# Optimization experiments

Hardware: AMD Instinct MI355X
Metric: run time of the kernel (lower is better)

The kernel has to match this reference:

```python
import jax, jax.numpy as jnp
from jax import lax
import numpy as np

B, T, I, H = 256, 512, 512, 1024

def setup_inputs() -> dict:
    key = jax.random.key(0)
    ks = jax.random.split(key, 6)
    s_ih = 1.0 / np.sqrt(H)
    return {
        "x": jax.random.normal(ks[0], (B, T, I), dtype=jnp.float32),
        "W_ih": jax.random.uniform(ks[1], (4 * H, I), minval=-s_ih, maxval=s_ih, dtype=jnp.float32),
        "W_hh": jax.random.uniform(ks[2], (4 * H, H), minval=-s_ih, maxval=s_ih, dtype=jnp.float32),
        "b_ih": jax.random.uniform(ks[3], (4 * H,), minval=-s_ih, maxval=s_ih, dtype=jnp.float32),
        "b_hh": jax.random.uniform(ks[4], (4 * H,), minval=-s_ih, maxval=s_ih, dtype=jnp.float32),
        "c0": jax.random.normal(ks[5], (B, H), dtype=jnp.float32),  # torch code inits cell state with randn
    }

def reference(x, W_ih, W_hh, b_ih, b_hh, c0):
    # Faithful to LSTMBody.forward: h0 = zeros, c0 = randn (provided as input),
    # per-step nn.LSTMCell; returns the final CELL state (the torch code's `out`).
    h0 = jnp.zeros((x.shape[0], W_hh.shape[1]), dtype=x.dtype)
    Wi_T = W_ih.T  # [I, 4H]
    Wh_T = W_hh.T  # [H, 4H]
    b = b_ih + b_hh

    def step(carry, xt):
        h, c = carry
        gates = xt @ Wi_T + h @ Wh_T + b  # [B, 4H]
        i, f, g, o = jnp.split(gates, 4, axis=-1)  # PyTorch gate order: i, f, g, o
        c_new = jax.nn.sigmoid(f) * c + jax.nn.sigmoid(i) * jnp.tanh(g)
        h_new = jax.nn.sigmoid(o) * jnp.tanh(c_new)
        return (h_new, c_new), None

    xs = jnp.swapaxes(x, 0, 1)  # [T, B, I] for scan over time
    (h, c), _ = lax.scan(step, (h0, c0), xs)
    return c
```

## Files before the change

### kernel.cpp

```cpp
#include <hip/hip_runtime.h>
#include <stdint.h>

#define Bsz 256
#define Tsz 512
#define Isz 512
#define Hsz 1024

typedef __attribute__((ext_vector_type(8))) short short8;
typedef __attribute__((ext_vector_type(4))) float f32x4;

static constexpr size_t XBF_OFF  = 0;
static constexpr size_t WIBF_OFF = 134217728;
static constexpr size_t HBUF_OFF = 138412032;
static constexpr size_t FLAG_OFF = 139460608;
static constexpr size_t WS_NEED  = 139493376;

__device__ __forceinline__ unsigned short f2bf(float f) {
  union { float f; unsigned u; } v; v.f = f;
  unsigned r = v.u + 0x7fff + ((v.u >> 16) & 1);
  return (unsigned short)(r >> 16);
}

__device__ __forceinline__ void cvt8(const float* __restrict__ s, unsigned short* __restrict__ d) {
  float4 a = *(const float4*)s;
  float4 b = *(const float4*)(s + 4);
  union { unsigned short us[8]; uint4 v; } o;
  o.us[0] = f2bf(a.x); o.us[1] = f2bf(a.y); o.us[2] = f2bf(a.z); o.us[3] = f2bf(a.w);
  o.us[4] = f2bf(b.x); o.us[5] = f2bf(b.y); o.us[6] = f2bf(b.z); o.us[7] = f2bf(b.w);
  *(uint4*)d = o.v;
}

__device__ __forceinline__ short8 ld_h(const unsigned short* p) {
  unsigned long long lo = __hip_atomic_load((unsigned long long*)(void*)p,
                                            __ATOMIC_RELAXED, __HIP_MEMORY_SCOPE_AGENT);
  unsigned long long hi = __hip_atomic_load((unsigned long long*)(void*)(p + 4),
                                            __ATOMIC_RELAXED, __HIP_MEMORY_SCOPE_AGENT);
  union { unsigned long long q[2]; short8 s; } u;
  u.q[0] = lo; u.q[1] = hi;
  return u.s;
}

__device__ __forceinline__ unsigned ld_flag(const unsigned* p) {
  return __hip_atomic_load((unsigned*)p, __ATOMIC_RELAXED, __HIP_MEMORY_SCOPE_AGENT);
}

__global__ __launch_bounds__(256)
void init_kernel(const float* __restrict__ x, const float* __restrict__ Wi,
                 unsigned char* __restrict__ ws)
{
  unsigned short* xbf  = (unsigned short*)(ws + XBF_OFF);
  unsigned short* wibf = (unsigned short*)(ws + WIBF_OFF);
  const int bid = blockIdx.x;
  const int tid = threadIdx.x;

  if (bid < 32768) {
    const int rowid = bid * 4 + (tid >> 6);
    const int t = rowid >> 8;
    const int b = rowid & 255;
    const int i = (tid & 63) * 8;
    const float* src = x + ((size_t)b * Tsz + t) * Isz + i;
    unsigned short* dst = xbf + (size_t)rowid * Isz + i;
    cvt8(src, dst);
  } else if (bid < 32768 + 1024) {
    const size_t base = (size_t)(bid - 32768) * 2048 + (size_t)tid * 8;
    cvt8(Wi + base, wibf + base);
  } else {
    const int z = bid - 33792;
    uint4 zero = make_uint4(0u, 0u, 0u, 0u);
    for (size_t j = (size_t)z * 256 + tid; j < 67584; j += (size_t)260 * 256)
      ((uint4*)(ws + HBUF_OFF))[j] = zero;
  }
}

__global__ __launch_bounds__(256, 1)
void lstm_persistent(const float* __restrict__ Wh,
                     const float* __restrict__ b_ih, const float* __restrict__ b_hh,
                     const float* __restrict__ c0, float* __restrict__ out,
                     unsigned char* __restrict__ ws)
{
  const unsigned short* __restrict__ xbf  = (const unsigned short*)(ws + XBF_OFF);
  const unsigned short* __restrict__ wibf = (const unsigned short*)(ws + WIBF_OFF);
  unsigned short* __restrict__ hbuf = (unsigned short*)(ws + HBUF_OFF);
  unsigned* __restrict__ flags = (unsigned*)(ws + FLAG_OFF);

  __shared__ unsigned short WhT[64][1032];
  __shared__ float bias[64];

  const int tid  = threadIdx.x;
  const int bid  = blockIdx.x;
  const int cg   = bid & 63;
  const int rg   = bid >> 6;
  const int wv   = tid >> 6;
  const int lane = tid & 63;
  const int l16  = lane & 15;
  const int quad = lane >> 4;

  {
    const int n  = tid >> 2;
    const int q  = n >> 4, u = n & 15;
    const int gc = q * 1024 + cg * 16 + u;
    const int k0 = (tid & 3) * 256;
    const float* src = Wh + (size_t)gc * Hsz + k0;
    unsigned short* dst = &WhT[n][k0];
    #pragma unroll 4
    for (int k = 0; k < 256; k += 8) cvt8(src + k, dst + k);
  }
  if (tid < 64) {
    const int q = tid >> 4, u = tid & 15;
    const int gc = q * 1024 + cg * 16 + u;
    bias[tid] = b_ih[gc] + b_hh[gc];
  }
  __syncthreads();

  const int rowbase = rg * 64 + wv * 16;
  const int arow    = rowbase + l16;
  const int hcol    = cg * 16 + l16;

  unsigned* const flag_base = flags + (size_t)rg * 2048 + (size_t)wv * 8;
  unsigned* const myslot    = flag_base + (size_t)cg * 32;
  unsigned* const pollp     = flag_base + (size_t)lane * 32;

  const float bi_r = bias[l16];
  const float bf_r = bias[16 + l16];
  const float bg_r = bias[32 + l16];
  const float bo_r = bias[48 + l16];

  float creg[4];
  #pragma unroll
  for (int r = 0; r < 4; ++r)
    creg[r] = c0[(size_t)(rowbase + quad * 4 + r) * Hsz + hcol];

  const unsigned short* bp[4];
  #pragma unroll
  for (int q = 0; q < 4; ++q)
    bp[q] = wibf + (size_t)(q * 1024 + cg * 16 + l16) * Isz + quad * 8;

  int p = 0;
  for (int t = 0; t < Tsz; ++t) {
    const unsigned short* xt = xbf  + (size_t)t * Bsz * Isz + (size_t)arow * Isz + quad * 8;
    const unsigned short* hp = hbuf + (size_t)p * Bsz * Hsz + (size_t)arow * Hsz + quad * 8;
    const unsigned tgt = (unsigned)t;

    f32x4 acc[4];
    #pragma unroll
    for (int q = 0; q < 4; ++q) acc[q] = (f32x4){0.f, 0.f, 0.f, 0.f};

    #pragma unroll 4
    for (int ks = 0; ks < 16; ++ks) {
      const int kk = ks * 32;
      short8 av = *(const short8*)(xt + kk);
      short8 b0 = *(const short8*)(bp[0] + kk);
      short8 b1 = *(const short8*)(bp[1] + kk);
      short8 b2 = *(const short8*)(bp[2] + kk);
      short8 b3 = *(const short8*)(bp[3] + kk);
      acc[0] = __builtin_amdgcn_mfma_f32_16x16x32_bf16(av, b0, acc[0], 0, 0, 0);
      acc[1] = __builtin_amdgcn_mfma_f32_16x16x32_bf16(av, b1, acc[1], 0, 0, 0);
      acc[2] = __builtin_amdgcn_mfma_f32_16x16x32_bf16(av, b2, acc[2], 0, 0, 0);
      acc[3] = __builtin_amdgcn_mfma_f32_16x16x32_bf16(av, b3, acc[3], 0, 0, 0);
    }

    if (t > 0) {
      unsigned v = ld_flag(pollp);
      while (!__all((int)(v >= tgt))) v = ld_flag(pollp);
      __atomic_signal_fence(__ATOMIC_SEQ_CST);
    }

    short8 hv[16];
    #pragma unroll
    for (int j = 0; j < 16; ++j) hv[j] = ld_h(hp + j * 32);

    #pragma unroll
    for (int ks = 0; ks < 32; ++ks) {
      short8 av = hv[ks & 15];
      if (ks + 16 < 32) hv[ks & 15] = ld_h(hp + (ks + 16) * 32);
      const int kk = ks * 32;
      short8 b0 = *(const short8*)(&WhT[l16     ][kk + quad * 8]);
      short8 b1 = *(const short8*)(&WhT[16 + l16][kk + quad * 8]);
      short8 b2 = *(const short8*)(&WhT[32 + l16][kk + quad * 8]);
      short8 b3 = *(const short8*)(&WhT[48 + l16][kk + quad * 8]);
      acc[0] = __builtin_amdgcn_mfma_f32_16x16x32_bf16(av, b0, acc[0], 0, 0, 0);
      acc[1] = __builtin_amdgcn_mfma_f32_16x16x32_bf16(av, b1, acc[1], 0, 0, 0);
      acc[2] = __builtin_amdgcn_mfma_f32_16x16x32_bf16(av, b2, acc[2], 0, 0, 0);
      acc[3] = __builtin_amdgcn_mfma_f32_16x16x32_bf16(av, b3, acc[3], 0, 0, 0);
    }

    unsigned short* hn = hbuf + (size_t)(p ^ 1) * Bsz * Hsz;
    #pragma unroll
    for (int r = 0; r < 4; ++r) {
      float gi = acc[0][r] + bi_r;
      float gf = acc[1][r] + bf_r;
      float gg = acc[2][r] + bg_r;
      float go = acc[3][r] + bo_r;
      float si = 1.f / (1.f + __expf(-gi));
      float sf = 1.f / (1.f + __expf(-gf));
      float tg = 1.f - 2.f / (__expf(2.f * gg) + 1.f);
      float so = 1.f / (1.f + __expf(-go));
      float cn = sf * creg[r] + si * tg;
      creg[r] = cn;
      float tc = 1.f - 2.f / (__expf(2.f * cn) + 1.f);
      __hip_atomic_store(&hn[(size_t)(rowbase + quad * 4 + r) * Hsz + hcol],
                         f2bf(so * tc), __ATOMIC_RELAXED, __HIP_MEMORY_SCOPE_AGENT);
    }

    asm volatile("s_waitcnt vmcnt(0)" ::: "memory");
    if (lane == 0)
      __hip_atomic_store(myslot, tgt + 1u, __ATOMIC_RELAXED, __HIP_MEMORY_SCOPE_AGENT);
    p ^= 1;
  }

  #pragma unroll
  for (int r = 0; r < 4; ++r)
    out[(size_t)(rowbase + quad * 4 + r) * Hsz + hcol] = creg[r];
}

extern "C" void kernel_launch(void* const* d_in, const int* in_sizes, int n_in,
                              void* d_out, int out_size, void* d_ws, size_t ws_size,
                              hipStream_t stream) {
  const float* x   = (const float*)d_in[0];
  const float* Wi  = (const float*)d_in[1];
  const float* Wh  = (const float*)d_in[2];
  const float* bih = (const float*)d_in[3];
  const float* bhh = (const float*)d_in[4];
  const float* c0  = (const float*)d_in[5];
  float* out = (float*)d_out;
  unsigned char* ws = (unsigned char*)d_ws;

  if (ws_size < WS_NEED) return;

  init_kernel<<<34052, 256, 0, stream>>>(x, Wi, ws);

  void* args[] = { (void*)&Wh, (void*)&bih, (void*)&bhh,
                   (void*)&c0, (void*)&out, (void*)&ws };
  hipLaunchCooperativeKernel((void*)lstm_persistent, dim3(256), dim3(256),
                             args, 0, stream);
}
```

Before: 9.934 ms.

## Split K dimension across two wave groups per block with LDS reduction

Doubles the block to 512 threads and has the second set of four waves handle the upper half of the K dimension for both the input and recurrent matmuls. Partial accumulators are reduced through shared memory, and only the first half then applies the gate nonlinearities, writes h and signals flags. This shortens the per-step serial MFMA chain inside the recurrence critical path. The cost is two block barriers per timestep plus extra LDS traffic and register pressure.

```diff
diff --git a/kernel.cpp b/kernel.cpp
--- a/kernel.cpp
+++ b/kernel.cpp
@@ -72,7 +72,7 @@
   }
 }
 
-__global__ __launch_bounds__(256, 1)
+__global__ __launch_bounds__(512, 2)
 void lstm_persistent(const float* __restrict__ Wh,
                      const float* __restrict__ b_ih, const float* __restrict__ b_hh,
                      const float* __restrict__ c0, float* __restrict__ out,
@@ -84,26 +84,29 @@
   unsigned* __restrict__ flags = (unsigned*)(ws + FLAG_OFF);
 
   __shared__ unsigned short WhT[64][1032];
+  __shared__ float red[4][64][17];
   __shared__ float bias[64];
 
   const int tid  = threadIdx.x;
   const int bid  = blockIdx.x;
   const int cg   = bid & 63;
   const int rg   = bid >> 6;
-  const int wv   = tid >> 6;
+  const int wv    = tid >> 6;
+  const int wv4   = wv & 3;
+  const int khalf = wv >> 2;
   const int lane = tid & 63;
   const int l16  = lane & 15;
   const int quad = lane >> 4;
 
   {
-    const int n  = tid >> 2;
+    const int n  = tid >> 3;
     const int q  = n >> 4, u = n & 15;
     const int gc = q * 1024 + cg * 16 + u;
-    const int k0 = (tid & 3) * 256;
+    const int k0 = (tid & 7) * 128;
     const float* src = Wh + (size_t)gc * Hsz + k0;
     unsigned short* dst = &WhT[n][k0];
     #pragma unroll 4
-    for (int k = 0; k < 256; k += 8) cvt8(src + k, dst + k);
+    for (int k = 0; k < 128; k += 8) cvt8(src + k, dst + k);
   }
   if (tid < 64) {
     const int q = tid >> 4, u = tid & 15;
@@ -112,41 +115,45 @@
   }
   __syncthreads();
 
-  const int rowbase = rg * 64 + wv * 16;
+  const int rowbase = rg * 64 + wv4 * 16;
   const int arow    = rowbase + l16;
   const int hcol    = cg * 16 + l16;
 
-  unsigned* const flag_base = flags + (size_t)rg * 2048 + (size_t)wv * 8;
+  unsigned* const flag_base = flags + (size_t)rg * 2048 + (size_t)wv4 * 8;
   unsigned* const myslot    = flag_base + (size_t)cg * 32;
-  unsigned* const pollp     = flag_base + (size_t)lane * 32;
+  unsigned* const pollp     = flag_base + (size_t)(khalf * 32 + (lane & 31)) * 32;
 
   const float bi_r = bias[l16];
   const float bf_r = bias[16 + l16];
   const float bg_r = bias[32 + l16];
   const float bo_r = bias[48 + l16];
 
-  float creg[4];
-  #pragma unroll
-  for (int r = 0; r < 4; ++r)
-    creg[r] = c0[(size_t)(rowbase + quad * 4 + r) * Hsz + hcol];
+  float creg[4] = {0.f, 0.f, 0.f, 0.f};
+  if (khalf == 0) {
+    #pragma unroll
+    for (int r = 0; r < 4; ++r)
+      creg[r] = c0[(size_t)(rowbase + quad * 4 + r) * Hsz + hcol];
+  }
 
   const unsigned short* bp[4];
   #pragma unroll
   for (int q = 0; q < 4; ++q)
-    bp[q] = wibf + (size_t)(q * 1024 + cg * 16 + l16) * Isz + quad * 8;
+    bp[q] = wibf + (size_t)(q * 1024 + cg * 16 + l16) * Isz + khalf * 256 + quad * 8;
 
   int p = 0;
   for (int t = 0; t < Tsz; ++t) {
-    const unsigned short* xt = xbf  + (size_t)t * Bsz * Isz + (size_t)arow * Isz + quad * 8;
-    const unsigned short* hp = hbuf + (size_t)p * Bsz * Hsz + (size_t)arow * Hsz + quad * 8;
+    const unsigned short* xt = xbf  + (size_t)t * Bsz * Isz + (size_t)arow * Isz
+                                    + khalf * 256 + quad * 8;
+    const unsigned short* hp = hbuf + (size_t)p * Bsz * Hsz + (size_t)arow * Hsz
+                                    + khalf * 512 + quad * 8;
     const unsigned tgt = (unsigned)t;
 
     f32x4 acc[4];
     #pragma unroll
     for (int q = 0; q < 4; ++q) acc[q] = (f32x4){0.f, 0.f, 0.f, 0.f};
 
-    #pragma unroll 4
-    for (int ks = 0; ks < 16; ++ks) {
+    #pragma unroll
+    for (int ks = 0; ks < 8; ++ks) {
       const int kk = ks * 32;
       short8 av = *(const short8*)(xt + kk);
       short8 b0 = *(const short8*)(bp[0] + kk);
@@ -165,15 +172,16 @@
       __atomic_signal_fence(__ATOMIC_SEQ_CST);
     }
 
-    short8 hv[16];
-    #pragma unroll
-    for (int j = 0; j < 16; ++j) hv[j] = ld_h(hp + j * 32);
-
-    #pragma unroll
-    for (int ks = 0; ks < 32; ++ks) {
-      short8 av = hv[ks & 15];
-      if (ks + 16 < 32) hv[ks & 15] = ld_h(hp + (ks + 16) * 32);
-      const int kk = ks * 32;
+    short8 hv[8];
+    #pragma unroll
+    for (int j = 0; j < 8; ++j) hv[j] = ld_h(hp + j * 32);
+
+    const int kbase = khalf * 512;
+    #pragma unroll
+    for (int ks = 0; ks < 16; ++ks) {
+      short8 av = hv[ks & 7];
+      if (ks + 8 < 16) hv[ks & 7] = ld_h(hp + (ks + 8) * 32);
+      const int kk = kbase + ks * 32;
       short8 b0 = *(const short8*)(&WhT[l16     ][kk + quad * 8]);
       short8 b1 = *(const short8*)(&WhT[16 + l16][kk + quad * 8]);
       short8 b2 = *(const short8*)(&WhT[32 + l16][kk + quad * 8]);
@@ -184,33 +192,54 @@
       acc[3] = __builtin_amdgcn_mfma_f32_16x16x32_bf16(av, b3, acc[3], 0, 0, 0);
     }
 
-    unsigned short* hn = hbuf + (size_t)(p ^ 1) * Bsz * Hsz;
-    #pragma unroll
-    for (int r = 0; r < 4; ++r) {
-      float gi = acc[0][r] + bi_r;
-      float gf = acc[1][r] + bf_r;
-      float gg = acc[2][r] + bg_r;
-      float go = acc[3][r] + bo_r;
-      float si = 1.f / (1.f + __expf(-gi));
-      float sf = 1.f / (1.f + __expf(-gf));
-      float tg = 1.f - 2.f / (__expf(2.f * gg) + 1.f);
-      float so = 1.f / (1.f + __expf(-go));
-      float cn = sf * creg[r] + si * tg;
-      creg[r] = cn;
-      float tc = 1.f - 2.f / (__expf(2.f * cn) + 1.f);
-      __hip_atomic_store(&hn[(size_t)(rowbase + quad * 4 + r) * Hsz + hcol],
-                         f2bf(so * tc), __ATOMIC_RELAXED, __HIP_MEMORY_SCOPE_AGENT);
-    }
-
-    asm volatile("s_waitcnt vmcnt(0)" ::: "memory");
-    if (lane == 0)
-      __hip_atomic_store(myslot, tgt + 1u, __ATOMIC_RELAXED, __HIP_MEMORY_SCOPE_AGENT);
+    if (khalf) {
+      #pragma unroll
+      for (int q = 0; q < 4; ++q)
+        #pragma unroll
+        for (int r = 0; r < 4; ++r)
+          red[wv4][lane][q * 4 + r] = acc[q][r];
+    }
+    __syncthreads();
+    if (!khalf) {
+      #pragma unroll
+      for (int q = 0; q < 4; ++q)
+        #pragma unroll
+        for (int r = 0; r < 4; ++r)
+          acc[q][r] += red[wv4][lane][q * 4 + r];
+    }
+    __syncthreads();
+
+    if (!khalf) {
+      unsigned short* hn = hbuf + (size_t)(p ^ 1) * Bsz * Hsz;
+      #pragma unroll
+      for (int r = 0; r < 4; ++r) {
+        float gi = acc[0][r] + bi_r;
+        float gf = acc[1][r] + bf_r;
+        float gg = acc[2][r] + bg_r;
+        float go = acc[3][r] + bo_r;
+        float si = 1.f / (1.f + __expf(-gi));
+        float sf = 1.f / (1.f + __expf(-gf));
+        float tg = 1.f - 2.f / (__expf(2.f * gg) + 1.f);
+        float so = 1.f / (1.f + __expf(-go));
+        float cn = sf * creg[r] + si * tg;
+        creg[r] = cn;
+        float tc = 1.f - 2.f / (__expf(2.f * cn) + 1.f);
+        __hip_atomic_store(&hn[(size_t)(rowbase + quad * 4 + r) * Hsz + hcol],
+                           f2bf(so * tc), __ATOMIC_RELAXED, __HIP_MEMORY_SCOPE_AGENT);
+      }
+
+      asm volatile("s_waitcnt vmcnt(0)" ::: "memory");
+      if (lane == 0)
+        __hip_atomic_store(myslot, tgt + 1u, __ATOMIC_RELAXED, __HIP_MEMORY_SCOPE_AGENT);
+    }
     p ^= 1;
   }
 
-  #pragma unroll
-  for (int r = 0; r < 4; ++r)
-    out[(size_t)(rowbase + quad * 4 + r) * Hsz + hcol] = creg[r];
+  if (khalf == 0) {
+    #pragma unroll
+    for (int r = 0; r < 4; ++r)
+      out[(size_t)(rowbase + quad * 4 + r) * Hsz + hcol] = creg[r];
+  }
 }
 
 extern "C" void kernel_launch(void* const* d_in, const int* in_sizes, int n_in,
@@ -231,6 +260,6 @@
 
   void* args[] = { (void*)&Wh, (void*)&bih, (void*)&bhh,
                    (void*)&c0, (void*)&out, (void*)&ws };
-  hipLaunchCooperativeKernel((void*)lstm_persistent, dim3(256), dim3(256),
+  hipLaunchCooperativeKernel((void*)lstm_persistent, dim3(256), dim3(512),
                              args, 0, stream);
 }
```

Measured after the change: 9.158 ms. 7.8% less time.
